# Kernel tuning notes

Hardware: AMD Instinct MI355X
Metric: run time of the kernel (lower is better)

## Reference

```python
import jax, jax.numpy as jnp
import numpy as np

NHEADS = 16
CAUSAL = True


def setup_inputs() -> dict:
    key = jax.random.key(0)
    k0, k1, k2, k3, k4 = jax.random.split(key, 5)
    B, S, E = 2, 2048, 1024
    x = jax.random.normal(k0, (B, S, E), dtype=jnp.float32)
    # torch nn.Linear weights: (out_features, in_features)
    w_in = jax.random.normal(k1, (3 * E, E), dtype=jnp.float32) * (E ** -0.5)
    b_in = jax.random.normal(k2, (3 * E,), dtype=jnp.float32) * 0.01
    w_out = jax.random.normal(k3, (E, E), dtype=jnp.float32) * (E ** -0.5)
    b_out = jax.random.normal(k4, (E,), dtype=jnp.float32) * 0.01
    return {"x": x, "w_in": w_in, "b_in": b_in, "w_out": w_out, "b_out": b_out}


def reference(x, w_in, b_in, w_out, b_out):
    B, S, E = x.shape
    H = NHEADS
    DK = E // H
    # fused qkv projection: (B,S,3E)
    qkv = x @ w_in.T + b_in
    q, k, v = jnp.split(qkv, 3, axis=-1)
    # (B,S,E) -> (B,H,S,DK)
    to_heads = lambda t: t.reshape(B, S, H, DK).transpose(0, 2, 1, 3)
    q, k, v = to_heads(q), to_heads(k), to_heads(v)
    # scores (B,H,S,S)
    w = jnp.einsum('bhqd,bhkd->bhqk', q, k)
    if CAUSAL:
        mask = jnp.triu(jnp.ones((S, S), dtype=bool), k=1)  # True above diagonal
        w = jnp.where(mask, -jnp.inf, w)
    w = w / jnp.sqrt(jnp.asarray(DK, dtype=w.dtype))
    w = jax.nn.softmax(w, axis=-1)
    out = jnp.einsum('bhqk,bhkd->bhqd', w, v)
    out = out.transpose(0, 2, 1, 3).reshape(B, S, E)
    return out @ w_out.T + b_out
```

## Files before the change

kernel.cpp:

```cpp
#include <hip/hip_runtime.h>
#include <hip/hip_bf16.h>
#include <stdint.h>


typedef __attribute__((ext_vector_type(4))) float f32x4;
typedef __attribute__((ext_vector_type(8))) __bf16 bf16x8;
typedef unsigned short u16;

#define LOG2E 1.4426950408889634f

__device__ __forceinline__ u16 f2bf(float f) {
  union { float f; uint32_t i; } v; v.f = f;
  return (u16)((v.i + 0x7fffu + ((v.i >> 16) & 1u)) >> 16);
}

__device__ __forceinline__ void gload_lds16(const u16* g, u16* l) {
  __builtin_amdgcn_global_load_lds((const __attribute__((address_space(1))) void*)g,
                                   (__attribute__((address_space(3))) void*)l, 16, 0, 0);
}

__device__ __forceinline__ bf16x8 ld_frag(const u16* ls, int row, int kh, int lane) {
  int sl = ((kh << 2) | (lane >> 4)) ^ (row & 7);
  return *(const bf16x8*)(ls + row * 64 + sl * 8);
}

__device__ __forceinline__ bf16x8 cvt8(f32x4 a, f32x4 b) {
  union { u16 u[8]; bf16x8 v; } o;
#pragma unroll
  for (int j = 0; j < 4; ++j) { o.u[j] = f2bf(a[j]); o.u[4 + j] = f2bf(b[j]); }
  return o.v;
}

__global__ __launch_bounds__(256) void cvt_f32_bf16(
    const float* __restrict__ in, u16* __restrict__ out, int n8) {
  int i = blockIdx.x * 256 + threadIdx.x;
  if (i >= n8) return;
  const f32x4* p = (const f32x4*)(in + (size_t)i * 8);
  *(bf16x8*)(out + (size_t)i * 8) = cvt8(p[0], p[1]);
}

template <int MODE, bool AF32, bool BF32>
__global__ __launch_bounds__(256, 2) void gemm_bt(
    const void* Ap, const void* Bp, const float* __restrict__ bias,
    void* out0, u16* __restrict__ out1, u16* __restrict__ out2, int K, int nbn) {
  __shared__ __align__(16) u16 lsA[2][128 * 64];
  __shared__ __align__(16) u16 lsB[2][128 * 64];
  const float* Af = (const float*)Ap; const u16* Ab = (const u16*)Ap;
  const float* Bf = (const float*)Bp; const u16* Bb = (const u16*)Bp;
  const int tid = threadIdx.x, lane = tid & 63, wid = tid >> 6;
  const int cpx = gridDim.x >> 3;
  const int wg = (blockIdx.x & 7) * cpx + (blockIdx.x >> 3);
  const int bm = wg / nbn, bn = wg % nbn;
  const int rowA0 = bm * 128, rowB0 = bn * 128;
  const int wm = wid >> 1, wn = wid & 1;

  f32x4 ra[4][2], rb[4][2];

  auto issue = [&](int buf, int k0) {
    if constexpr (AF32) {
#pragma unroll
      for (int i = 0; i < 4; ++i) {
        int u = i * 256 + tid, r = u >> 3, s = u & 7;
        const float* p = Af + (size_t)(rowA0 + r) * K + k0 + s * 8;
        ra[i][0] = *(const f32x4*)p; ra[i][1] = *(const f32x4*)(p + 4);
      }
    } else {
#pragma unroll
      for (int i = 0; i < 4; ++i) {
        int u = i * 256 + tid, r = u >> 3, s = u & 7;
        int gk = k0 + ((s ^ (r & 7)) << 3);
        gload_lds16(Ab + (size_t)(rowA0 + r) * K + gk,
                    &lsA[buf][(i * 256 + wid * 64) << 3]);
      }
    }
    if constexpr (BF32) {
#pragma unroll
      for (int i = 0; i < 4; ++i) {
        int u = i * 256 + tid, r = u >> 3, s = u & 7;
        const float* p = Bf + (size_t)(rowB0 + r) * K + k0 + s * 8;
        rb[i][0] = *(const f32x4*)p; rb[i][1] = *(const f32x4*)(p + 4);
      }
    } else {
#pragma unroll
      for (int i = 0; i < 4; ++i) {
        int u = i * 256 + tid, r = u >> 3, s = u & 7;
        int gk = k0 + ((s ^ (r & 7)) << 3);
        gload_lds16(Bb + (size_t)(rowB0 + r) * K + gk,
                    &lsB[buf][(i * 256 + wid * 64) << 3]);
      }
    }
  };
  auto commit = [&](int buf) {
    if constexpr (AF32) {
#pragma unroll
      for (int i = 0; i < 4; ++i) {
        int u = i * 256 + tid, r = u >> 3, s = u & 7;
        *(bf16x8*)&lsA[buf][r * 64 + ((s ^ (r & 7)) << 3)] = cvt8(ra[i][0], ra[i][1]);
      }
    }
    if constexpr (BF32) {
#pragma unroll
      for (int i = 0; i < 4; ++i) {
        int u = i * 256 + tid, r = u >> 3, s = u & 7;
        *(bf16x8*)&lsB[buf][r * 64 + ((s ^ (r & 7)) << 3)] = cvt8(rb[i][0], rb[i][1]);
      }
    }
  };

  f32x4 acc[4][4] = {};
  const int NT = K >> 6;
  issue(0, 0);
  commit(0);
  asm volatile("s_waitcnt vmcnt(0)" ::: "memory");
  __syncthreads();
  int cur = 0;
  for (int t = 0; t < NT; ++t) {
    if (t + 1 < NT) issue(cur ^ 1, (t + 1) << 6);
    const u16* la = lsA[cur];
    const u16* lb = lsB[cur];
    bf16x8 af[4][2], bf[4][2];
#pragma unroll
    for (int m = 0; m < 4; ++m) {
      int row = wm * 64 + m * 16 + (lane & 15);
#pragma unroll
      for (int kh = 0; kh < 2; ++kh) af[m][kh] = ld_frag(la, row, kh, lane);
    }
#pragma unroll
    for (int n = 0; n < 4; ++n) {
      int row = wn * 64 + n * 16 + (lane & 15);
#pragma unroll
      for (int kh = 0; kh < 2; ++kh) bf[n][kh] = ld_frag(lb, row, kh, lane);
    }
#pragma unroll
    for (int m = 0; m < 4; ++m)
#pragma unroll
      for (int n = 0; n < 4; ++n)
#pragma unroll
        for (int kh = 0; kh < 2; ++kh)
          acc[m][n] = __builtin_amdgcn_mfma_f32_16x16x32_bf16(af[m][kh], bf[n][kh], acc[m][n], 0, 0, 0);
    if (t + 1 < NT) commit(cur ^ 1);
    __syncthreads();
    cur ^= 1;
  }

#pragma unroll
  for (int m = 0; m < 4; ++m) {
    int gRow0 = rowA0 + wm * 64 + m * 16 + ((lane >> 4) << 2);
#pragma unroll
    for (int n = 0; n < 4; ++n) {
      int gCol = rowB0 + wn * 64 + n * 16 + (lane & 15);
      float bv = bias[gCol];
      if (MODE == 0) {
        int sec = gCol >> 10, e = gCol & 1023;
        int h = e >> 6, d = e & 63;
        int b = gRow0 >> 11, s0 = gRow0 & 2047;
        int bh = b * 16 + h;
        if (sec == 2) {
          union { u16 u[4]; uint64_t q; } pk;
#pragma unroll
          for (int r = 0; r < 4; ++r) pk.u[r] = f2bf(acc[m][n][r] + bv);
          *(uint64_t*)&out2[((size_t)bh * 64 + d) * 2048 + s0] = pk.q;
        } else {
          u16* dst = (sec == 0) ? (u16*)out0 : out1;
#pragma unroll
          for (int r = 0; r < 4; ++r)
            dst[((size_t)bh * 2048 + (s0 + r)) * 64 + d] = f2bf(acc[m][n][r] + bv);
        }
      } else {
        float* O = (float*)out0;
#pragma unroll
        for (int r = 0; r < 4; ++r)
          O[(size_t)(gRow0 + r) * 1024 + gCol] = acc[m][n][r] + bv;
      }
    }
  }
}

__global__ __launch_bounds__(256, 4) void attn_kernel(
    const u16* __restrict__ Q, const u16* __restrict__ Kt,
    const u16* __restrict__ VT, u16* __restrict__ attn) {
  __shared__ __align__(16) u16 lsK[2][64 * 64];
  __shared__ __align__(16) u16 lsV[2][64 * 64];
  __shared__ __align__(16) u16 lsP[64 * 64];
  const int tid = threadIdx.x, lane = tid & 63, wid = tid >> 6;
  const int idx = blockIdx.x;
  const int qt = 31 - (idx >> 5);
  const int bh = idx & 31;
  const int b = bh >> 4, h = bh & 15;
  const u16* Qb = Q + (size_t)bh * 2048 * 64;
  const u16* Kb = Kt + (size_t)bh * 2048 * 64;
  const u16* Vb = VT + (size_t)bh * 64 * 2048;
  const int qRow0 = qt * 64 + wid * 16;

  bf16x8 qf[2];
#pragma unroll
  for (int kh = 0; kh < 2; ++kh) {
    int row = qRow0 + (lane & 15);
    int d0 = kh * 32 + ((lane >> 4) << 3);
    qf[kh] = *(const bf16x8*)(Qb + (size_t)row * 64 + d0);
  }

  float rowmax[4], rowsum[4];
  f32x4 acc_o[4] = {};
#pragma unroll
  for (int r = 0; r < 4; ++r) { rowmax[r] = -1e30f; rowsum[r] = 0.f; }

  auto stageKV = [&](int buf, int kt) {
#pragma unroll
    for (int i = 0; i < 2; ++i) {
      int u = i * 256 + tid, r = u >> 3, s = u & 7;
      int gk = ((s ^ (r & 7)) << 3);
      gload_lds16(Kb + (size_t)(kt * 64 + r) * 64 + gk,
                  &lsK[buf][(i * 256 + wid * 64) << 3]);
    }
#pragma unroll
    for (int i = 0; i < 2; ++i) {
      int u = i * 256 + tid, r = u >> 3, s = u & 7;
      int gk = kt * 64 + ((s ^ (r & 7)) << 3);
      gload_lds16(Vb + (size_t)r * 2048 + gk,
                  &lsV[buf][(i * 256 + wid * 64) << 3]);
    }
  };

  const int NT = qt + 1;
  stageKV(0, 0);
  asm volatile("s_waitcnt vmcnt(0)" ::: "memory");
  __syncthreads();
  int cur = 0;
  for (int kt = 0; kt < NT; ++kt) {
    if (kt + 1 < NT) stageKV(cur ^ 1, kt + 1);

    f32x4 sc[4] = {};
    bf16x8 kf[4][2];
#pragma unroll
    for (int n = 0; n < 4; ++n) {
      int row = n * 16 + (lane & 15);
#pragma unroll
      for (int kh = 0; kh < 2; ++kh) kf[n][kh] = ld_frag(lsK[cur], row, kh, lane);
    }
#pragma unroll
    for (int n = 0; n < 4; ++n)
#pragma unroll
      for (int kh = 0; kh < 2; ++kh)
        sc[n] = __builtin_amdgcn_mfma_f32_16x16x32_bf16(qf[kh], kf[n][kh], sc[n], 0, 0, 0);

    const bool maskTile = (kt == qt);
    float tmax[4];
#pragma unroll
    for (int r = 0; r < 4; ++r) tmax[r] = -1e30f;
#pragma unroll
    for (int n = 0; n < 4; ++n)
#pragma unroll
      for (int r = 0; r < 4; ++r) {
        float s = sc[n][r] * 0.125f;
        if (maskTile) {
          int qrow = qRow0 + ((lane >> 4) << 2) + r;
          int kcol = kt * 64 + n * 16 + (lane & 15);
          if (kcol > qrow) s = -1e30f;
        }
        sc[n][r] = s;
        tmax[r] = fmaxf(tmax[r], s);
      }
#pragma unroll
    for (int r = 0; r < 4; ++r) {
      float v = tmax[r];
      v = fmaxf(v, __shfl_xor(v, 1));
      v = fmaxf(v, __shfl_xor(v, 2));
      v = fmaxf(v, __shfl_xor(v, 4));
      v = fmaxf(v, __shfl_xor(v, 8));
      tmax[r] = v;
    }

    float psum[4] = {0.f, 0.f, 0.f, 0.f};
#pragma unroll
    for (int r = 0; r < 4; ++r) {
      float mnew = fmaxf(rowmax[r], tmax[r]);
      float rs = exp2f((rowmax[r] - mnew) * LOG2E);
      rowmax[r] = mnew;
      rowsum[r] *= rs;
#pragma unroll
      for (int n = 0; n < 4; ++n) acc_o[n][r] *= rs;
    }
#pragma unroll
    for (int n = 0; n < 4; ++n)
#pragma unroll
      for (int r = 0; r < 4; ++r) {
        float p = exp2f((sc[n][r] - rowmax[r]) * LOG2E);
        psum[r] += p;
        int rowl = wid * 16 + ((lane >> 4) << 2) + r;
        int col = n * 16 + (lane & 15);
        int sl = (col >> 3) ^ (rowl & 7);
        lsP[rowl * 64 + sl * 8 + (col & 7)] = f2bf(p);
      }
#pragma unroll
    for (int r = 0; r < 4; ++r) {
      float v = psum[r];
      v += __shfl_xor(v, 1); v += __shfl_xor(v, 2);
      v += __shfl_xor(v, 4); v += __shfl_xor(v, 8);
      rowsum[r] += v;
    }

    bf16x8 pf[2], vf[4][2];
#pragma unroll
    for (int n = 0; n < 4; ++n) {
      int row = n * 16 + (lane & 15);
#pragma unroll
      for (int kh = 0; kh < 2; ++kh) vf[n][kh] = ld_frag(lsV[cur], row, kh, lane);
    }
#pragma unroll
    for (int kh = 0; kh < 2; ++kh)
      pf[kh] = ld_frag(lsP, wid * 16 + (lane & 15), kh, lane);
#pragma unroll
    for (int n = 0; n < 4; ++n)
#pragma unroll
      for (int kh = 0; kh < 2; ++kh)
        acc_o[n] = __builtin_amdgcn_mfma_f32_16x16x32_bf16(pf[kh], vf[n][kh], acc_o[n], 0, 0, 0);

    __syncthreads();
    cur ^= 1;
  }

#pragma unroll
  for (int r = 0; r < 4; ++r) {
    float inv = 1.0f / rowsum[r];
    int srow = qt * 64 + wid * 16 + ((lane >> 4) << 2) + r;
#pragma unroll
    for (int n = 0; n < 4; ++n) {
      int d = n * 16 + (lane & 15);
      attn[((size_t)(b * 2048 + srow)) * 1024 + h * 64 + d] = f2bf(acc_o[n][r] * inv);
    }
  }
}

extern "C" void kernel_launch(void* const* d_in, const int* in_sizes, int n_in,
                              void* d_out, int out_size, void* d_ws, size_t ws_size,
                              hipStream_t stream) {
  const float* x     = (const float*)d_in[0];
  const float* w_in  = (const float*)d_in[1];
  const float* b_in  = (const float*)d_in[2];
  const float* w_out = (const float*)d_in[3];
  const float* b_out = (const float*)d_in[4];
  float* out = (float*)d_out;
  u16* ws = (u16*)d_ws;

  const size_t PH = (size_t)32 * 2048 * 64;
  const size_t NW_IN = (size_t)3072 * 1024;
  const size_t NW_OUT = (size_t)1024 * 1024;
  const size_t need_big = (4 * PH + NW_IN + NW_OUT) * sizeof(u16);

  u16* Qw  = ws;
  u16* Kw  = ws + PH;
  u16* VTw = ws + 2 * PH;
  u16* Aw  = ws + 3 * PH;

  if (ws_size >= need_big) {
    u16* xbf = Aw;
    u16* wibf = ws + 4 * PH;
    u16* wobf = wibf + NW_IN;
    cvt_f32_bf16<<<dim3((int)(PH / 8 / 256)), 256, 0, stream>>>(x, xbf, (int)(PH / 8));
    cvt_f32_bf16<<<dim3((int)(NW_IN / 8 / 256)), 256, 0, stream>>>(w_in, wibf, (int)(NW_IN / 8));
    cvt_f32_bf16<<<dim3((int)(NW_OUT / 8 / 256)), 256, 0, stream>>>(w_out, wobf, (int)(NW_OUT / 8));
    gemm_bt<0, false, false><<<dim3(768), 256, 0, stream>>>(xbf, wibf, b_in, Qw, Kw, VTw, 1024, 24);
    attn_kernel<<<dim3(1024), 256, 0, stream>>>(Qw, Kw, VTw, Aw);
    gemm_bt<1, false, false><<<dim3(256), 256, 0, stream>>>(Aw, wobf, b_out, out, nullptr, nullptr, 1024, 8);
  } else {
    if (ws_size < 4 * PH * sizeof(u16)) return;
    gemm_bt<0, true, true><<<dim3(768), 256, 0, stream>>>(x, w_in, b_in, Qw, Kw, VTw, 1024, 24);
    attn_kernel<<<dim3(1024), 256, 0, stream>>>(Qw, Kw, VTw, Aw);
    gemm_bt<1, false, true><<<dim3(256), 256, 0, stream>>>(Aw, w_out, b_out, out, nullptr, nullptr, 1024, 8);
  }
}
```

Baseline: 216.0 us.

## Fold softmax scale into Q, transpose score MFMA, merge conversion kernels

Folds the 1/sqrt(dk)*log2e factor into the Q projection epilogue, so the attention loop no longer multiplies scores before exp2. It swaps the MFMA operands so each lane holds one query row, which reduces the row max and sum reductions to two cross-lane shuffles. P is written to LDS as packed 64-bit stores into a per-wave slice. It also merges the three f32-to-bf16 conversion launches into one, uses the hardware bf16 conversion, and reorders the attention block to query-tile mapping for better causal load balance. Rounding Q after scaling changes numerics slightly, and the remapping adds extra shuffles to broadcast the rescale factors.

```diff
diff --git a/kernel.cpp b/kernel.cpp
--- a/kernel.cpp
+++ b/kernel.cpp
@@ -7,11 +7,11 @@
 typedef __attribute__((ext_vector_type(8))) __bf16 bf16x8;
 typedef unsigned short u16;
 
-#define LOG2E 1.4426950408889634f
+#define QSCALE 0.18033688011112042f
 
 __device__ __forceinline__ u16 f2bf(float f) {
-  union { float f; uint32_t i; } v; v.f = f;
-  return (u16)((v.i + 0x7fffu + ((v.i >> 16) & 1u)) >> 16);
+  __bf16 h = (__bf16)f;
+  union { __bf16 b; u16 u; } c; c.b = h; return c.u;
 }
 
 __device__ __forceinline__ void gload_lds16(const u16* g, u16* l) {
@@ -31,12 +31,19 @@
   return o.v;
 }
 
-__global__ __launch_bounds__(256) void cvt_f32_bf16(
-    const float* __restrict__ in, u16* __restrict__ out, int n8) {
+__global__ __launch_bounds__(256) void cvt_all(
+    const float* __restrict__ x, const float* __restrict__ wi,
+    const float* __restrict__ wo,
+    u16* __restrict__ xb, u16* __restrict__ wib, u16* __restrict__ wob,
+    int n1, int n2, int n3) {
   int i = blockIdx.x * 256 + threadIdx.x;
-  if (i >= n8) return;
-  const f32x4* p = (const f32x4*)(in + (size_t)i * 8);
-  *(bf16x8*)(out + (size_t)i * 8) = cvt8(p[0], p[1]);
+  const float* src; u16* dst; int off;
+  if (i < n1) { src = x; dst = xb; off = i; }
+  else if (i < n1 + n2) { src = wi; dst = wib; off = i - n1; }
+  else if (i < n1 + n2 + n3) { src = wo; dst = wob; off = i - n1 - n2; }
+  else return;
+  const f32x4* p = (const f32x4*)(src + (size_t)off * 8);
+  *(bf16x8*)(dst + (size_t)off * 8) = cvt8(p[0], p[1]);
 }
 
 template <int MODE, bool AF32, bool BF32>
@@ -160,11 +167,15 @@
 #pragma unroll
           for (int r = 0; r < 4; ++r) pk.u[r] = f2bf(acc[m][n][r] + bv);
           *(uint64_t*)&out2[((size_t)bh * 64 + d) * 2048 + s0] = pk.q;
+        } else if (sec == 0) {
+#pragma unroll
+          for (int r = 0; r < 4; ++r)
+            ((u16*)out0)[((size_t)bh * 2048 + (s0 + r)) * 64 + d] =
+                f2bf((acc[m][n][r] + bv) * QSCALE);
         } else {
-          u16* dst = (sec == 0) ? (u16*)out0 : out1;
 #pragma unroll
           for (int r = 0; r < 4; ++r)
-            dst[((size_t)bh * 2048 + (s0 + r)) * 64 + d] = f2bf(acc[m][n][r] + bv);
+            out1[((size_t)bh * 2048 + (s0 + r)) * 64 + d] = f2bf(acc[m][n][r] + bv);
         }
       } else {
         float* O = (float*)out0;
@@ -184,26 +195,27 @@
   __shared__ __align__(16) u16 lsP[64 * 64];
   const int tid = threadIdx.x, lane = tid & 63, wid = tid >> 6;
   const int idx = blockIdx.x;
-  const int qt = 31 - (idx >> 5);
-  const int bh = idx & 31;
+  const int jj = idx & 31, a = jj >> 2, bsel = jj & 3;
+  const int qt = (bsel == 0) ? 31 - a : (bsel == 1) ? a : (bsel == 2) ? 15 - a : 16 + a;
+  const int bh = idx >> 5;
   const int b = bh >> 4, h = bh & 15;
   const u16* Qb = Q + (size_t)bh * 2048 * 64;
   const u16* Kb = Kt + (size_t)bh * 2048 * 64;
   const u16* Vb = VT + (size_t)bh * 64 * 2048;
   const int qRow0 = qt * 64 + wid * 16;
+  const int g = lane >> 4;
+  const int qloc = lane & 15;
 
   bf16x8 qf[2];
 #pragma unroll
   for (int kh = 0; kh < 2; ++kh) {
-    int row = qRow0 + (lane & 15);
-    int d0 = kh * 32 + ((lane >> 4) << 3);
+    int row = qRow0 + qloc;
+    int d0 = kh * 32 + (g << 3);
     qf[kh] = *(const bf16x8*)(Qb + (size_t)row * 64 + d0);
   }
 
-  float rowmax[4], rowsum[4];
+  float rowmax = -1e30f, rowsum = 0.f;
   f32x4 acc_o[4] = {};
-#pragma unroll
-  for (int r = 0; r < 4; ++r) { rowmax[r] = -1e30f; rowsum[r] = 0.f; }
 
   auto stageKV = [&](int buf, int kt) {
 #pragma unroll
@@ -221,6 +233,8 @@
                   &lsV[buf][(i * 256 + wid * 64) << 3]);
     }
   };
+
+  u16* lsPw = lsP + wid * 1024;
 
   const int NT = qt + 1;
   stageKV(0, 0);
@@ -234,7 +248,7 @@
     bf16x8 kf[4][2];
 #pragma unroll
     for (int n = 0; n < 4; ++n) {
-      int row = n * 16 + (lane & 15);
+      int row = n * 16 + qloc;
 #pragma unroll
       for (int kh = 0; kh < 2; ++kh) kf[n][kh] = ld_frag(lsK[cur], row, kh, lane);
     }
@@ -242,74 +256,66 @@
     for (int n = 0; n < 4; ++n)
 #pragma unroll
       for (int kh = 0; kh < 2; ++kh)
-        sc[n] = __builtin_amdgcn_mfma_f32_16x16x32_bf16(qf[kh], kf[n][kh], sc[n], 0, 0, 0);
-
-    const bool maskTile = (kt == qt);
-    float tmax[4];
-#pragma unroll
-    for (int r = 0; r < 4; ++r) tmax[r] = -1e30f;
+        sc[n] = __builtin_amdgcn_mfma_f32_16x16x32_bf16(kf[n][kh], qf[kh], sc[n], 0, 0, 0);
+
+    if (kt == qt) {
+      int qrow = qRow0 + qloc;
+#pragma unroll
+      for (int n = 0; n < 4; ++n)
+#pragma unroll
+        for (int r = 0; r < 4; ++r) {
+          int kcol = kt * 64 + n * 16 + (g << 2) + r;
+          if (kcol > qrow) sc[n][r] = -1e30f;
+        }
+    }
+
+    float tmax = sc[0][0];
 #pragma unroll
     for (int n = 0; n < 4; ++n)
 #pragma unroll
+      for (int r = 0; r < 4; ++r) tmax = fmaxf(tmax, sc[n][r]);
+    tmax = fmaxf(tmax, __shfl_xor(tmax, 16));
+    tmax = fmaxf(tmax, __shfl_xor(tmax, 32));
+
+    float mnew = fmaxf(rowmax, tmax);
+    float rs = exp2f(rowmax - mnew);
+    rowmax = mnew;
+
+    float psum = 0.f;
+#pragma unroll
+    for (int n = 0; n < 4; ++n) {
+      union { u16 u[4]; uint64_t q; } pk;
+#pragma unroll
       for (int r = 0; r < 4; ++r) {
-        float s = sc[n][r] * 0.125f;
-        if (maskTile) {
-          int qrow = qRow0 + ((lane >> 4) << 2) + r;
-          int kcol = kt * 64 + n * 16 + (lane & 15);
-          if (kcol > qrow) s = -1e30f;
-        }
-        sc[n][r] = s;
-        tmax[r] = fmaxf(tmax[r], s);
-      }
-#pragma unroll
-    for (int r = 0; r < 4; ++r) {
-      float v = tmax[r];
-      v = fmaxf(v, __shfl_xor(v, 1));
-      v = fmaxf(v, __shfl_xor(v, 2));
-      v = fmaxf(v, __shfl_xor(v, 4));
-      v = fmaxf(v, __shfl_xor(v, 8));
-      tmax[r] = v;
-    }
-
-    float psum[4] = {0.f, 0.f, 0.f, 0.f};
-#pragma unroll
-    for (int r = 0; r < 4; ++r) {
-      float mnew = fmaxf(rowmax[r], tmax[r]);
-      float rs = exp2f((rowmax[r] - mnew) * LOG2E);
-      rowmax[r] = mnew;
-      rowsum[r] *= rs;
-#pragma unroll
-      for (int n = 0; n < 4; ++n) acc_o[n][r] *= rs;
-    }
+        float p = exp2f(sc[n][r] - mnew);
+        psum += p;
+        pk.u[r] = f2bf(p);
+      }
+      int sl = ((n << 1) | (g >> 1)) ^ (qloc & 7);
+      *(uint64_t*)&lsPw[qloc * 64 + (sl << 3) + ((g & 1) << 2)] = pk.q;
+    }
+    psum += __shfl_xor(psum, 16);
+    psum += __shfl_xor(psum, 32);
+    rowsum = rowsum * rs + psum;
+
+    float rsq[4];
+#pragma unroll
+    for (int r = 0; r < 4; ++r) rsq[r] = __shfl(rs, (g << 2) + r);
 #pragma unroll
     for (int n = 0; n < 4; ++n)
 #pragma unroll
-      for (int r = 0; r < 4; ++r) {
-        float p = exp2f((sc[n][r] - rowmax[r]) * LOG2E);
-        psum[r] += p;
-        int rowl = wid * 16 + ((lane >> 4) << 2) + r;
-        int col = n * 16 + (lane & 15);
-        int sl = (col >> 3) ^ (rowl & 7);
-        lsP[rowl * 64 + sl * 8 + (col & 7)] = f2bf(p);
-      }
-#pragma unroll
-    for (int r = 0; r < 4; ++r) {
-      float v = psum[r];
-      v += __shfl_xor(v, 1); v += __shfl_xor(v, 2);
-      v += __shfl_xor(v, 4); v += __shfl_xor(v, 8);
-      rowsum[r] += v;
-    }
+      for (int r = 0; r < 4; ++r) acc_o[n][r] *= rsq[r];
 
     bf16x8 pf[2], vf[4][2];
 #pragma unroll
     for (int n = 0; n < 4; ++n) {
-      int row = n * 16 + (lane & 15);
+      int row = n * 16 + qloc;
 #pragma unroll
       for (int kh = 0; kh < 2; ++kh) vf[n][kh] = ld_frag(lsV[cur], row, kh, lane);
     }
 #pragma unroll
     for (int kh = 0; kh < 2; ++kh)
-      pf[kh] = ld_frag(lsP, wid * 16 + (lane & 15), kh, lane);
+      pf[kh] = ld_frag(lsPw, qloc, kh, lane);
 #pragma unroll
     for (int n = 0; n < 4; ++n)
 #pragma unroll
@@ -320,14 +326,17 @@
     cur ^= 1;
   }
 
+  float inv = 1.0f / rowsum;
+  float invq[4];
+#pragma unroll
+  for (int r = 0; r < 4; ++r) invq[r] = __shfl(inv, (g << 2) + r);
 #pragma unroll
   for (int r = 0; r < 4; ++r) {
-    float inv = 1.0f / rowsum[r];
-    int srow = qt * 64 + wid * 16 + ((lane >> 4) << 2) + r;
-#pragma unroll
-    for (int n = 0; n < 4; ++n) {
-      int d = n * 16 + (lane & 15);
-      attn[((size_t)(b * 2048 + srow)) * 1024 + h * 64 + d] = f2bf(acc_o[n][r] * inv);
+    int srow = qRow0 + (g << 2) + r;
+#pragma unroll
+    for (int n = 0; n < 4; ++n) {
+      int d = n * 16 + qloc;
+      attn[((size_t)(b * 2048 + srow)) * 1024 + h * 64 + d] = f2bf(acc_o[n][r] * invq[r]);
     }
   }
 }
@@ -357,9 +366,8 @@
     u16* xbf = Aw;
     u16* wibf = ws + 4 * PH;
     u16* wobf = wibf + NW_IN;
-    cvt_f32_bf16<<<dim3((int)(PH / 8 / 256)), 256, 0, stream>>>(x, xbf, (int)(PH / 8));
-    cvt_f32_bf16<<<dim3((int)(NW_IN / 8 / 256)), 256, 0, stream>>>(w_in, wibf, (int)(NW_IN / 8));
-    cvt_f32_bf16<<<dim3((int)(NW_OUT / 8 / 256)), 256, 0, stream>>>(w_out, wobf, (int)(NW_OUT / 8));
+    cvt_all<<<dim3(4096), 256, 0, stream>>>(x, w_in, w_out, xbf, wibf, wobf,
+                                            (int)(PH / 8), (int)(NW_IN / 8), (int)(NW_OUT / 8));
     gemm_bt<0, false, false><<<dim3(768), 256, 0, stream>>>(xbf, wibf, b_in, Qw, Kw, VTw, 1024, 24);
     attn_kernel<<<dim3(1024), 256, 0, stream>>>(Qw, Kw, VTw, Aw);
     gemm_bt<1, false, false><<<dim3(256), 256, 0, stream>>>(Aw, wobf, b_out, out, nullptr, nullptr, 1024, 8);
```

After: 218.8 us. No clear change (+1.3%).
